# Performance work log

Hardware: AMD Instinct MI355X
Metric: run time of the kernel (lower is better)

## Reference

```python
import jax, jax.numpy as jnp
import numpy as np

K = 5          # kernel_size per pseudo-dim
KK = K * K     # 25 weight slots (dim=2)
NUM_GRAPHS = 64


def spline_conv(x, src, dst, pseudo, W, root, bias):
    """SplineConv, degree-1 open B-spline, dim=2, aggr='mean', root weight + bias.
    x: [N, I], pseudo: [E, 2] in [0,1], W: [KK, I, O], root: [I, O], bias: [O].
    """
    N = x.shape[0]
    E = src.shape[0]
    O = W.shape[-1]
    # degree-1 open spline: v = u * (K-1); linear interpolation between knots
    v = pseudo * (K - 1)                      # [E, 2]
    bot = jnp.floor(v)
    frac = v - bot                            # [E, 2]
    bot = bot.astype(jnp.int32)
    # precompute per-node transform for every kernel slot: [N, KK, O] -> flat [N*KK, O]
    Xk = jnp.einsum('ni,kio->nko', x, W).reshape(N * KK, O)
    msg = jnp.zeros((E, O), x.dtype)
    for s0 in (0, 1):
        b0 = frac[:, 0] if s0 else 1.0 - frac[:, 0]
        i0 = jnp.clip(bot[:, 0] + s0, 0, K - 1)
        for s1 in (0, 1):
            b1 = frac[:, 1] if s1 else 1.0 - frac[:, 1]
            i1 = jnp.clip(bot[:, 1] + s1, 0, K - 1)
            flat = src * KK + i0 * K + i1     # [E] gather index into Xk
            msg = msg + (b0 * b1)[:, None] * Xk[flat]
    # mean aggregation over incoming edges
    agg = jax.ops.segment_sum(msg, dst, num_segments=N)
    deg = jax.ops.segment_sum(jnp.ones((E,), x.dtype), dst, num_segments=N)
    agg = agg / jnp.maximum(deg, 1.0)[:, None]
    return agg + x @ root + bias


def batch_average(x, batch, num_graphs):
    s = jax.ops.segment_sum(x, batch, num_segments=num_graphs)
    c = jax.ops.segment_sum(jnp.ones((x.shape[0],), x.dtype), batch, num_segments=num_graphs)
    return s / jnp.maximum(c, 1.0)[:, None]


def setup_inputs() -> dict:
    key = jax.random.key(0)
    ks = jax.random.split(key, 16)
    N, E = 30000, 600000
    x = jax.random.normal(ks[0], (N, 8), dtype=jnp.float32)
    edge_index = jax.random.randint(ks[1], (2, E), 0, N, dtype=jnp.int64)
    pseudo = jax.random.uniform(ks[2], (E, 2), dtype=jnp.float32)
    batch = jnp.sort(jax.random.randint(ks[3], (N,), 0, NUM_GRAPHS, dtype=jnp.int64))

    def glorot(k, shape):
        fan = shape[-2] + shape[-1]
        return jax.random.normal(k, shape, dtype=jnp.float32) * np.sqrt(2.0 / fan)

    return {
        'x': x, 'edge_index': edge_index, 'pseudo': pseudo, 'batch': batch,
        'W1': glorot(ks[4], (KK, 8, 32)),   'root1': glorot(ks[5], (8, 32)),   'b1': jnp.zeros((32,), jnp.float32),
        'W2': glorot(ks[6], (KK, 32, 64)),  'root2': glorot(ks[7], (32, 64)),  'b2': jnp.zeros((64,), jnp.float32),
        'W3': glorot(ks[8], (KK, 64, 124)), 'root3': glorot(ks[9], (64, 124)), 'b3': jnp.zeros((124,), jnp.float32),
        'fc_w': glorot(ks[10], (124, 30)),  'fc_b': jnp.zeros((30,), jnp.float32),
    }


def reference(x, edge_index, pseudo, batch,
              W1, root1, b1, W2, root2, b2, W3, root3, b3, fc_w, fc_b):
    src = edge_index[0].astype(jnp.int32)
    dst = edge_index[1].astype(jnp.int32)
    batch32 = batch.astype(jnp.int32)
    h = jax.nn.elu(spline_conv(x, src, dst, pseudo, W1, root1, b1))
    h = jax.nn.elu(spline_conv(h, src, dst, pseudo, W2, root2, b2))
    h = jax.nn.elu(spline_conv(h, src, dst, pseudo, W3, root3, b3))
    g = batch_average(h, batch32, NUM_GRAPHS)        # [G, 124]
    # dropout is identity in eval mode
    logits = g @ fc_w + fc_b                         # [G, 30]
    return jax.nn.log_softmax(logits, axis=-1)
```

## Files before the change

kernel.cpp:

```cpp
#include <hip/hip_runtime.h>
#include <cstdint>
#include <cstddef>

#define KKSLOTS 25

typedef __attribute__((ext_vector_type(8))) short short8;
typedef __attribute__((ext_vector_type(4))) float f32x4;
typedef __attribute__((ext_vector_type(4))) unsigned short us4;

__device__ __forceinline__ unsigned short f2bf(float f) {
    unsigned u = __float_as_uint(f);
    u += 0x7FFF + ((u >> 16) & 1);
    return (unsigned short)(u >> 16);
}
__device__ __forceinline__ float bf2f(unsigned short b) {
    return __uint_as_float((unsigned)b << 16);
}

__global__ void csr_count_kernel(const int* __restrict__ dst, int* __restrict__ cnt, int E) {
    int e = blockIdx.x * blockDim.x + threadIdx.x;
    if (e < E) atomicAdd(&cnt[dst[e]], 1);
}

#define SCAN_B 256
__global__ __launch_bounds__(SCAN_B) void scan1_kernel(const int* __restrict__ cnt,
                                                       int* __restrict__ off,
                                                       int* __restrict__ bsum, int N) {
    __shared__ int tmp[SCAN_B];
    int g = blockIdx.x * SCAN_B + threadIdx.x;
    int v = (g < N) ? cnt[g] : 0;
    tmp[threadIdx.x] = v;
    __syncthreads();
    for (int d = 1; d < SCAN_B; d <<= 1) {
        int t = (threadIdx.x >= d) ? tmp[threadIdx.x - d] : 0;
        __syncthreads();
        tmp[threadIdx.x] += t;
        __syncthreads();
    }
    if (g < N) off[g] = tmp[threadIdx.x] - v;
    if (threadIdx.x == SCAN_B - 1) bsum[blockIdx.x] = tmp[threadIdx.x];
}

__global__ __launch_bounds__(SCAN_B) void scan2_kernel(int* __restrict__ bsum, int nb) {
    __shared__ int tmp[SCAN_B];
    int v = (threadIdx.x < nb) ? bsum[threadIdx.x] : 0;
    tmp[threadIdx.x] = v;
    __syncthreads();
    for (int d = 1; d < SCAN_B; d <<= 1) {
        int t = (threadIdx.x >= d) ? tmp[threadIdx.x - d] : 0;
        __syncthreads();
        tmp[threadIdx.x] += t;
        __syncthreads();
    }
    if (threadIdx.x < nb) bsum[threadIdx.x] = tmp[threadIdx.x] - v;
}

__global__ void scan3_kernel(int* __restrict__ off, const int* __restrict__ bsum, int N) {
    int g = blockIdx.x * SCAN_B + threadIdx.x;
    if (g < N) off[g] += bsum[blockIdx.x];
}

__global__ void csr_fill_kernel(const int* __restrict__ src, const int* __restrict__ dst,
                                const float* __restrict__ pseudo,
                                int* __restrict__ off, int4* __restrict__ rec, int E) {
    int e = blockIdx.x * blockDim.x + threadIdx.x;
    if (e >= E) return;
    int d = dst[e];
    int p = atomicAdd(&off[d], 1);
    float v0 = pseudo[2 * e + 0] * 4.0f;
    float v1 = pseudo[2 * e + 1] * 4.0f;
    float fl0 = floorf(v0), fl1 = floorf(v1);
    float f0 = v0 - fl0, f1 = v1 - fl1;
    int i0 = min(max((int)fl0, 0), 3);
    int i1 = min(max((int)fl1, 0), 3);
    int4 r;
    r.x = src[e];
    r.y = i0 | (i1 << 8);
    r.z = __float_as_int(f0);
    r.w = __float_as_int(f1);
    rec[p] = r;
}

__global__ void to_bf16_kernel(const float* __restrict__ in, unsigned short* __restrict__ out, int n) {
    int i = blockIdx.x * 256 + threadIdx.x;
    if (i < n) out[i] = f2bf(in[i]);
}

template<int KP, int I, int O, int OP>
__global__ void build_wt_kernel(const float* __restrict__ W, const float* __restrict__ root,
                                unsigned short* __restrict__ WT) {
    int idx = blockIdx.x * 256 + threadIdx.x;
    if (idx >= OP * KP) return;
    int o = idx / KP, k = idx - o * KP;
    float v = 0.0f;
    if (o < O) {
        if (k < KKSLOTS * I) v = W[(size_t)k * O + o];
        else if (k < (KKSLOTS + 1) * I) v = root[(size_t)(k - KKSLOTS * I) * O + o];
    }
    WT[idx] = f2bf(v);
}

template<int I, int KP>
__global__ __launch_bounds__(256) void seg_accum_kernel(
        const unsigned short* __restrict__ xb, const int4* __restrict__ rec,
        const int* __restrict__ off, unsigned short* __restrict__ accB,
        int nlo, int nhi) {
    constexpr int SLOTS = KKSLOTS * I;
    constexpr int EPW = 64 / I;
    int wline = threadIdx.x >> 6, lane = threadIdx.x & 63;
    int wid = blockIdx.x * 4 + wline;
    int nwt = gridDim.x << 2;

    int e_lo = (nlo == 0) ? 0 : off[nlo - 1];
    int e_hi = off[nhi - 1];
    long long span = (long long)e_hi - e_lo;
    int t0 = e_lo + (int)(span * wid / nwt);
    int t1 = e_lo + (int)(span * (wid + 1) / nwt);

    int ns, ne;
    {   int lo = nlo, hi = nhi;
        while (lo < hi) { int m = (lo + hi) >> 1; if (off[m] > t0) hi = m; else lo = m + 1; }
        ns = (wid == 0) ? nlo : lo; }
    {   int lo = nlo, hi = nhi;
        while (lo < hi) { int m = (lo + hi) >> 1; if (off[m] > t1) hi = m; else lo = m + 1; }
        ne = (wid == nwt - 1) ? nhi : lo; }
    if (ns >= ne) return;

    int h  = lane / I;
    int ch = lane % I;

    float acc[5][5];
    #pragma unroll
    for (int r = 0; r < 5; ++r)
        #pragma unroll
        for (int c = 0; c < 5; ++c) acc[r][c] = 0.0f;

    int j = (ns == 0) ? 0 : off[ns - 1];
    for (int n = ns; n < ne; ++n) {
        int je = off[n];
        int jstart = j;
        for (; j < je; j += EPW) {
            int idx = j + h;
            int cl = min(idx, je - 1);
            int4 r = rec[cl];
            float scale = (idx < je) ? 1.0f : 0.0f;
            float f0 = __int_as_float(r.z), f1 = __int_as_float(r.w);
            float g0 = 1.0f - f0, g1 = 1.0f - f1;
            int i0 = r.y & 0xFF, i1 = (r.y >> 8) & 0xFF;
            float xv = bf2f(xb[(size_t)r.x * I + ch]) * scale;
            float w1v[5], p0[5];
            #pragma unroll
            for (int c = 0; c < 5; ++c)
                w1v[c] = (c == i1) ? g1 : ((c == i1 + 1) ? f1 : 0.0f);
            #pragma unroll
            for (int rr = 0; rr < 5; ++rr)
                p0[rr] = ((rr == i0) ? g0 : ((rr == i0 + 1) ? f0 : 0.0f)) * xv;
            #pragma unroll
            for (int rr = 0; rr < 5; ++rr)
                #pragma unroll
                for (int c = 0; c < 5; ++c)
                    acc[rr][c] = fmaf(p0[rr], w1v[c], acc[rr][c]);
        }
        j = je;

        float dinv = 1.0f / fmaxf((float)(je - jstart), 1.0f);
        unsigned short* drow = accB + (size_t)(n - nlo) * KP;
        #pragma unroll
        for (int rr = 0; rr < 5; ++rr) {
            #pragma unroll
            for (int c = 0; c < 5; ++c) {
                float v = acc[rr][c];
                if constexpr (EPW > 1) {
                    #pragma unroll
                    for (int s = I; s < 64; s <<= 1) v += __shfl_xor(v, s, 64);
                }
                if (lane < I) drow[(rr * 5 + c) * I + ch] = f2bf(v * dinv);
                acc[rr][c] = 0.0f;
            }
        }
        if (lane < I) drow[SLOTS + ch] = xb[(size_t)n * I + ch];
        if constexpr (KP > SLOTS + I) {
            if (lane < KP - SLOTS - I) drow[SLOTS + I + lane] = 0;
        }
    }
}

template<int KP, int O, int OP>
__global__ __launch_bounds__(256) void contract_mfma_kernel(
        const unsigned short* __restrict__ accB, const unsigned short* __restrict__ WT,
        const float* __restrict__ bias, unsigned short* __restrict__ hout,
        int nlo, int nhi) {
    constexpr int NF = OP / 16;
    constexpr int LDW = 40;
    __shared__ unsigned short wTl[OP][LDW];
    int tid = threadIdx.x;
    int wv = tid >> 6, lane = tid & 63;
    int quad = lane >> 4, l16 = lane & 15;
    int n0 = nlo + blockIdx.x * 64;

    int an = n0 + wv * 16 + l16;
    int arow = min(an, nhi - 1) - nlo;

    f32x4 acc[NF];
    #pragma unroll
    for (int t = 0; t < NF; ++t) acc[t] = (f32x4){0.0f, 0.0f, 0.0f, 0.0f};

    for (int k0 = 0; k0 < KP; k0 += 32) {
        for (int t = tid; t < OP * 8; t += 256) {
            int o = t >> 3;
            int kk = (t & 7) * 4;
            *(us4*)&wTl[o][kk] = *(const us4*)&WT[(size_t)o * KP + k0 + kk];
        }
        __syncthreads();
        short8 a = *(const short8*)(accB + (size_t)arow * KP + k0 + quad * 8);
        #pragma unroll
        for (int t = 0; t < NF; ++t) {
            short8 b = *(const short8*)&wTl[t * 16 + l16][quad * 8];
            acc[t] = __builtin_amdgcn_mfma_f32_16x16x32_bf16(a, b, acc[t], 0, 0, 0);
        }
        __syncthreads();
    }

    #pragma unroll
    for (int t = 0; t < NF; ++t) {
        int o = t * 16 + l16;
        if (o >= O) continue;
        float bs = bias[o];
        #pragma unroll
        for (int r = 0; r < 4; ++r) {
            int n = n0 + wv * 16 + quad * 4 + r;
            if (n >= nhi) continue;
            float v = acc[t][r] + bs;
            v = (v > 0.0f) ? v : expm1f(v);
            hout[(size_t)n * O + o] = f2bf(v);
        }
    }
}

#define GS_CH 128
__global__ __launch_bounds__(128) void graph_reduce_kernel(
        const unsigned short* __restrict__ h3, const int* __restrict__ batch,
        float* __restrict__ g, float* __restrict__ cnt, int N) {
    int o = threadIdx.x;
    int n0 = blockIdx.x * GS_CH;
    int n1 = min(n0 + GS_CH, N);
    if (o < 124) {
        float local = 0.0f;
        int cur_b = batch[n0];
        for (int n = n0; n < n1; ++n) {
            int b = batch[n];
            if (b != cur_b) {
                atomicAdd(&g[cur_b * 124 + o], local);
                local = 0.0f;
                cur_b = b;
            }
            local += bf2f(h3[(size_t)n * 124 + o]);
        }
        atomicAdd(&g[cur_b * 124 + o], local);
    } else if (o == 124) {
        float localc = 0.0f;
        int cur_b = batch[n0];
        for (int n = n0; n < n1; ++n) {
            int b = batch[n];
            if (b != cur_b) {
                atomicAdd(&cnt[cur_b], localc);
                localc = 0.0f;
                cur_b = b;
            }
            localc += 1.0f;
        }
        atomicAdd(&cnt[cur_b], localc);
    }
}

__global__ void head_kernel(const float* __restrict__ g, const float* __restrict__ cnt,
                            const float* __restrict__ fcw, const float* __restrict__ fcb,
                            float* __restrict__ out) {
    __shared__ float logits[32];
    __shared__ float red[2];
    int b = blockIdx.x;
    int o = threadIdx.x;
    float c = fmaxf(cnt[b], 1.0f);
    if (o < 30) {
        float a = fcb[o];
        for (int i = 0; i < 124; ++i)
            a = fmaf(g[b * 124 + i] / c, fcw[i * 30 + o], a);
        logits[o] = a;
    }
    __syncthreads();
    if (o == 0) {
        float m = -1e30f;
        for (int j = 0; j < 30; ++j) m = fmaxf(m, logits[j]);
        float s = 0.0f;
        for (int j = 0; j < 30; ++j) s += expf(logits[j] - m);
        red[0] = m;
        red[1] = logf(s);
    }
    __syncthreads();
    if (o < 30) out[b * 30 + o] = logits[o] - red[0] - red[1];
}

template<int I, int O, int OP>
static void run_layer(const unsigned short* hb, const unsigned short* WT, const float* bias,
                      unsigned short* hout, unsigned short* accB,
                      const int4* rec, const int* off,
                      int N, size_t avail, hipStream_t stream) {
    constexpr int KP = ((26 * I + 31) / 32) * 32;
    size_t perNode = (size_t)KP * 2;
    size_t maxNodesS = avail / perNode;
    int maxNodes = (maxNodesS > (size_t)N) ? N : (int)maxNodesS;
    if (maxNodes < 64) maxNodes = 64;
    for (int nlo = 0; nlo < N; nlo += maxNodes) {
        int nhi = nlo + maxNodes;
        if (nhi > N) nhi = N;
        int cn = nhi - nlo;
        seg_accum_kernel<I, KP><<<2048, 256, 0, stream>>>(hb, rec, off, accB, nlo, nhi);
        contract_mfma_kernel<KP, O, OP><<<(cn + 63) / 64, 256, 0, stream>>>(
            accB, WT, bias, hout, nlo, nhi);
    }
}

extern "C" void kernel_launch(void* const* d_in, const int* in_sizes, int n_in,
                              void* d_out, int out_size, void* d_ws, size_t ws_size,
                              hipStream_t stream) {
    const float* x      = (const float*)d_in[0];
    const int*   ei     = (const int*)  d_in[1];
    const float* pseudo = (const float*)d_in[2];
    const int*   batch  = (const int*)  d_in[3];
    const float* W1 = (const float*)d_in[4];
    const float* r1 = (const float*)d_in[5];
    const float* b1 = (const float*)d_in[6];
    const float* W2 = (const float*)d_in[7];
    const float* r2 = (const float*)d_in[8];
    const float* b2 = (const float*)d_in[9];
    const float* W3 = (const float*)d_in[10];
    const float* r3 = (const float*)d_in[11];
    const float* b3 = (const float*)d_in[12];
    const float* fcw = (const float*)d_in[13];
    const float* fcb = (const float*)d_in[14];

    int N = in_sizes[0] / 8;
    int E = in_sizes[1] / 2;
    const int* srcp = ei;
    const int* dstp = ei + E;

    constexpr int KP1 = 224, KP2 = 832, KP3 = 1664;

    char* p = (char*)d_ws;
    unsigned short* xb  = (unsigned short*)p; p += (size_t)N * 8 * 2;
    unsigned short* h1  = (unsigned short*)p; p += (size_t)N * 32 * 2;
    unsigned short* h2  = (unsigned short*)p; p += (size_t)N * 64 * 2;
    unsigned short* h3  = (unsigned short*)p; p += (size_t)N * 124 * 2;
    float* gbuf = (float*)p; p += 64 * 124 * 4;
    float* cntF = (float*)p; p += 256;
    int*   cntI = (int*)p;   p += ((size_t)N * 4 + 15) & ~15ULL;
    int*   off  = (int*)p;   p += ((size_t)N * 4 + 15) & ~15ULL;
    int*   bsum = (int*)p;   p += SCAN_B * 4;
    int4*  rec  = (int4*)p;  p += (size_t)E * 16;
    unsigned short* WT1 = (unsigned short*)p; p += (size_t)32  * KP1 * 2;
    unsigned short* WT2 = (unsigned short*)p; p += (size_t)64  * KP2 * 2;
    unsigned short* WT3 = (unsigned short*)p; p += (size_t)128 * KP3 * 2;
    unsigned short* accB = (unsigned short*)p;
    size_t used = (size_t)(p - (char*)d_ws);
    size_t avail = (ws_size > used) ? (ws_size - used) : 0;

    hipMemsetAsync(gbuf, 0, 64 * 124 * 4 + 256 + (((size_t)N * 4 + 15) & ~15ULL), stream);

    int nb_scan = (N + SCAN_B - 1) / SCAN_B;
    csr_count_kernel<<<(E + 255) / 256, 256, 0, stream>>>(dstp, cntI, E);
    scan1_kernel<<<nb_scan, SCAN_B, 0, stream>>>(cntI, off, bsum, N);
    scan2_kernel<<<1, SCAN_B, 0, stream>>>(bsum, nb_scan);
    scan3_kernel<<<nb_scan, SCAN_B, 0, stream>>>(off, bsum, N);
    csr_fill_kernel<<<(E + 255) / 256, 256, 0, stream>>>(srcp, dstp, pseudo, off, rec, E);

    to_bf16_kernel<<<(N * 8 + 255) / 256, 256, 0, stream>>>(x, xb, N * 8);
    build_wt_kernel<KP1, 8,  32,  32 ><<<(32  * KP1 + 255) / 256, 256, 0, stream>>>(W1, r1, WT1);
    build_wt_kernel<KP2, 32, 64,  64 ><<<(64  * KP2 + 255) / 256, 256, 0, stream>>>(W2, r2, WT2);
    build_wt_kernel<KP3, 64, 124, 128><<<(128 * KP3 + 255) / 256, 256, 0, stream>>>(W3, r3, WT3);

    run_layer<8,  32,  32 >(xb, WT1, b1, h1, accB, rec, off, N, avail, stream);
    run_layer<32, 64,  64 >(h1, WT2, b2, h2, accB, rec, off, N, avail, stream);
    run_layer<64, 124, 128>(h2, WT3, b3, h3, accB, rec, off, N, avail, stream);

    graph_reduce_kernel<<<(N + GS_CH - 1) / GS_CH, 128, 0, stream>>>(h3, batch, gbuf, cntF, N);
    head_kernel<<<64, 64, 0, stream>>>(gbuf, cntF, fcw, fcb, (float*)d_out);
}
```

Baseline: 538.5 us.

## Accumulate spline slots via LDS atomics instead of 25 register FMAs per edge

Replaces the per-lane 5x5 register accumulator, which needed 25 FMAs per edge plus a shuffle reduction per node, with a per-wave LDS buffer updated by four atomic adds at the edge's flattened slot index. Edge records are batched so several rec and x loads are in flight at once, and the record now stores a precomputed flat slot index. Write-out packs two bf16 values per store. The cost is LDS atomic contention, since lanes within a wave that share a channel can hit the same address, and extra LDS zeroing per node.

```diff
diff --git a/kernel.cpp b/kernel.cpp
--- a/kernel.cpp
+++ b/kernel.cpp
@@ -75,7 +75,7 @@
     int i1 = min(max((int)fl1, 0), 3);
     int4 r;
     r.x = src[e];
-    r.y = i0 | (i1 << 8);
+    r.y = i0 * 5 + i1;
     r.z = __float_as_int(f0);
     r.w = __float_as_int(f1);
     rec[p] = r;
@@ -107,7 +107,10 @@
         int nlo, int nhi) {
     constexpr int SLOTS = KKSLOTS * I;
     constexpr int EPW = 64 / I;
+    constexpr int BATCH = (I == 8) ? 2 : 4;
+    __shared__ float la_all[4][SLOTS];
     int wline = threadIdx.x >> 6, lane = threadIdx.x & 63;
+    float* la = la_all[wline];
     int wid = blockIdx.x * 4 + wline;
     int nwt = gridDim.x << 2;
 
@@ -129,59 +132,65 @@
     int h  = lane / I;
     int ch = lane % I;
 
-    float acc[5][5];
-    #pragma unroll
-    for (int r = 0; r < 5; ++r)
-        #pragma unroll
-        for (int c = 0; c < 5; ++c) acc[r][c] = 0.0f;
+    for (int t = lane; t < SLOTS; t += 64) la[t] = 0.0f;
 
     int j = (ns == 0) ? 0 : off[ns - 1];
     for (int n = ns; n < ne; ++n) {
         int je = off[n];
         int jstart = j;
-        for (; j < je; j += EPW) {
+        while (j + BATCH * EPW <= je) {
+            int4 r[BATCH];
+            float xv[BATCH];
+            #pragma unroll
+            for (int u = 0; u < BATCH; ++u) r[u] = rec[j + h + u * EPW];
+            #pragma unroll
+            for (int u = 0; u < BATCH; ++u) xv[u] = bf2f(xb[(size_t)r[u].x * I + ch]);
+            #pragma unroll
+            for (int u = 0; u < BATCH; ++u) {
+                float f0 = __int_as_float(r[u].z), f1 = __int_as_float(r[u].w);
+                float g0 = 1.0f - f0, g1 = 1.0f - f1;
+                float* base = &la[r[u].y * I + ch];
+                unsafeAtomicAdd(base,         g0 * g1 * xv[u]);
+                unsafeAtomicAdd(base + I,     g0 * f1 * xv[u]);
+                unsafeAtomicAdd(base + 5 * I, f0 * g1 * xv[u]);
+                unsafeAtomicAdd(base + 6 * I, f0 * f1 * xv[u]);
+            }
+            j += BATCH * EPW;
+        }
+        while (j < je) {
             int idx = j + h;
-            int cl = min(idx, je - 1);
-            int4 r = rec[cl];
-            float scale = (idx < je) ? 1.0f : 0.0f;
-            float f0 = __int_as_float(r.z), f1 = __int_as_float(r.w);
-            float g0 = 1.0f - f0, g1 = 1.0f - f1;
-            int i0 = r.y & 0xFF, i1 = (r.y >> 8) & 0xFF;
-            float xv = bf2f(xb[(size_t)r.x * I + ch]) * scale;
-            float w1v[5], p0[5];
-            #pragma unroll
-            for (int c = 0; c < 5; ++c)
-                w1v[c] = (c == i1) ? g1 : ((c == i1 + 1) ? f1 : 0.0f);
-            #pragma unroll
-            for (int rr = 0; rr < 5; ++rr)
-                p0[rr] = ((rr == i0) ? g0 : ((rr == i0 + 1) ? f0 : 0.0f)) * xv;
-            #pragma unroll
-            for (int rr = 0; rr < 5; ++rr)
-                #pragma unroll
-                for (int c = 0; c < 5; ++c)
-                    acc[rr][c] = fmaf(p0[rr], w1v[c], acc[rr][c]);
+            if (idx < je) {
+                int4 r = rec[idx];
+                float f0 = __int_as_float(r.z), f1 = __int_as_float(r.w);
+                float g0 = 1.0f - f0, g1 = 1.0f - f1;
+                float xv = bf2f(xb[(size_t)r.x * I + ch]);
+                float* base = &la[r.y * I + ch];
+                unsafeAtomicAdd(base,         g0 * g1 * xv);
+                unsafeAtomicAdd(base + I,     g0 * f1 * xv);
+                unsafeAtomicAdd(base + 5 * I, f0 * g1 * xv);
+                unsafeAtomicAdd(base + 6 * I, f0 * f1 * xv);
+            }
+            j += EPW;
         }
         j = je;
 
+        __builtin_amdgcn_s_waitcnt(0);
         float dinv = 1.0f / fmaxf((float)(je - jstart), 1.0f);
-        unsigned short* drow = accB + (size_t)(n - nlo) * KP;
-        #pragma unroll
-        for (int rr = 0; rr < 5; ++rr) {
-            #pragma unroll
-            for (int c = 0; c < 5; ++c) {
-                float v = acc[rr][c];
-                if constexpr (EPW > 1) {
-                    #pragma unroll
-                    for (int s = I; s < 64; s <<= 1) v += __shfl_xor(v, s, 64);
-                }
-                if (lane < I) drow[(rr * 5 + c) * I + ch] = f2bf(v * dinv);
-                acc[rr][c] = 0.0f;
-            }
-        }
-        if (lane < I) drow[SLOTS + ch] = xb[(size_t)n * I + ch];
-        if constexpr (KP > SLOTS + I) {
-            if (lane < KP - SLOTS - I) drow[SLOTS + I + lane] = 0;
-        }
+        unsigned* drow = (unsigned*)(accB + (size_t)(n - nlo) * KP);
+        const unsigned* hrow = (const unsigned*)(xb + (size_t)n * I);
+        for (int t = lane; t < KP / 2; t += 64) {
+            int e0 = 2 * t;
+            unsigned outv;
+            if (e0 < SLOTS) {
+                float v0 = la[e0] * dinv, v1 = la[e0 + 1] * dinv;
+                outv = (unsigned)f2bf(v0) | ((unsigned)f2bf(v1) << 16);
+            } else {
+                int ii = e0 - SLOTS;
+                outv = (ii < I) ? hrow[ii >> 1] : 0u;
+            }
+            drow[t] = outv;
+        }
+        for (int t = lane; t < SLOTS; t += 64) la[t] = 0.0f;
     }
 }
 
```

New measurement: 1.637 ms. 204% more time.
